# Performance work log

Measured on AMD Instinct MI355X. Metric: run time of the kernel, lower is better.

## Reference

```python
import jax, jax.numpy as jnp
import numpy as np

N_NODES = 100000
N_EDGES = 3200000  # avg degree 32
EPS = 1e-12


def setup_inputs() -> dict:
    key = jax.random.key(0)
    k1, k2, k3, k4, k5 = jax.random.split(key, 5)
    positions = jax.random.normal(k1, (N_NODES, 3), dtype=jnp.float32)
    node_feat = jnp.ones((N_NODES, 1), dtype=jnp.float32)  # dummy 1x0e data
    w0 = jax.random.normal(k2, (1,), dtype=jnp.float32)    # linear weight for 0e output
    w1 = jax.random.normal(k3, (3,), dtype=jnp.float32)    # linear weight for 1o output (elementwise)
    edge_src = jax.random.randint(k4, (N_EDGES,), 0, N_NODES, dtype=jnp.int32)
    edge_dst = jax.random.randint(k5, (N_EDGES,), 0, N_NODES, dtype=jnp.int32)
    return {"positions": positions, "node_feat": node_feat, "w0": w0, "w1": w1,
            "edge_src": edge_src, "edge_dst": edge_dst}


def reference(positions, node_feat, w0, w1, edge_src, edge_dst):
    n_nodes = positions.shape[0]
    # relative positions per edge: dest - src  [E,3]
    rel = positions[edge_dst] - positions[edge_src]
    # spherical harmonics lmax=1: Y0 = 1 (constant 0e), Y1 = unit direction (1o)
    norm = jnp.sqrt(jnp.sum(rel * rel, axis=-1, keepdims=True))
    sh1 = rel / jnp.maximum(norm, EPS)                      # [E,3]
    # gather dest-node scalar feature (code gathers dest_node_feat)
    s = node_feat[edge_dst]                                 # [E,1]
    # tensor product of 0e scalar with (0e + 1o): tp0 = s*1, tp1 = s*sh1
    # LinearLayer: elementwise multiply by per-irrep weight vectors
    out0 = w0 * s                                           # [E,1]
    out1 = w1 * (s * sh1)                                   # [E,3]
    edge_out = jnp.concatenate([out0, out1], axis=-1)       # [E,4]
    # scatter-mean aggregation over incoming edges per dest node
    sums = jax.ops.segment_sum(edge_out, edge_dst, num_segments=n_nodes)
    ones = jnp.ones((edge_out.shape[0], 1), dtype=edge_out.dtype)
    counts = jax.ops.segment_sum(ones, edge_dst, num_segments=n_nodes)
    return sums / jnp.maximum(counts, 1.0)                  # [N,4]
```

## Files before the change

### kernel.cpp

```cpp
#include <hip/hip_runtime.h>


#define EPS 1e-12f
#define FSCALE 128.0f
#define FBIAS 128
#define CHUNK_SHIFT 13
#define CHUNK 8192
#define NCHUNK_MAX 16
#define BLKA 512
#define TPA 4
#define BLKB 512
#define SUBS 39

__device__ __forceinline__ void sh_fields(const float* __restrict__ pos,
                                          int s, int d,
                                          unsigned& fx, unsigned& fy, unsigned& fz) {
    float rx = pos[3 * d + 0] - pos[3 * s + 0];
    float ry = pos[3 * d + 1] - pos[3 * s + 1];
    float rz = pos[3 * d + 2] - pos[3 * s + 2];
    float nrm = sqrtf(rx * rx + ry * ry + rz * rz);
    float inv = 1.0f / fmaxf(nrm, EPS);
    fx = (unsigned)(FBIAS + (int)rintf(rx * inv * FSCALE));
    fy = (unsigned)(FBIAS + (int)rintf(ry * inv * FSCALE));
    fz = (unsigned)(FBIAS + (int)rintf(rz * inv * FSCALE));
}

__global__ __launch_bounds__(BLKA) void phaseA(
        const float* __restrict__ pos,
        const int* __restrict__ dst,
        const int* __restrict__ src,
        unsigned* __restrict__ gcnt,
        unsigned long long* __restrict__ recs,
        int n_edges, int cap, int n_chunk) {
    __shared__ unsigned h[NCHUNK_MAX];
    __shared__ unsigned base[NCHUNK_MAX];
    int tid = threadIdx.x;
    if (tid < n_chunk) h[tid] = 0;
    __syncthreads();

    long e0 = (long)blockIdx.x * (BLKA * TPA);
    unsigned long long rec[TPA];
    int ch[TPA];
    unsigned rank[TPA];
    bool val[TPA];
#pragma unroll
    for (int t = 0; t < TPA; ++t) {
        long j = e0 + (long)t * BLKA + tid;
        val[t] = (j < n_edges);
        if (val[t]) {
            int d = dst[j];
            int s = src[j];
            unsigned fx, fy, fz;
            sh_fields(pos, s, d, fx, fy, fz);
            ch[t] = d >> CHUNK_SHIFT;
            unsigned local = (unsigned)d & (CHUNK - 1);
            rec[t] = ((unsigned long long)local << 27)
                   | ((unsigned long long)fx << 18)
                   | ((unsigned long long)fy << 9)
                   | (unsigned long long)fz;
            rank[t] = atomicAdd(&h[ch[t]], 1u);
        }
    }
    __syncthreads();
    if (tid < n_chunk) base[tid] = h[tid] ? atomicAdd(&gcnt[tid], h[tid]) : 0u;
    __syncthreads();
#pragma unroll
    for (int t = 0; t < TPA; ++t) {
        if (val[t]) {
            unsigned idx = base[ch[t]] + rank[t];
            if (idx < (unsigned)cap)
                recs[(size_t)ch[t] * (unsigned)cap + idx] = rec[t];
        }
    }
}

__global__ __launch_bounds__(BLKB) void phaseB(
        const unsigned* __restrict__ gcnt,
        const unsigned long long* __restrict__ recs,
        unsigned long long* __restrict__ accR,
        int cap, int n_chunk, int padded) {
    __shared__ unsigned long long lds[CHUNK];
    int c   = (int)blockIdx.x % n_chunk;
    int sub = (int)blockIdx.x / n_chunk;
    unsigned cnt = gcnt[c];
    if (cnt > (unsigned)cap) cnt = (unsigned)cap;

    for (int i = threadIdx.x; i < CHUNK; i += BLKB) lds[i] = 0ull;
    __syncthreads();

    const unsigned long long* bucket = recs + (size_t)c * (unsigned)cap;
    for (unsigned j = sub * BLKB + threadIdx.x; j < cnt; j += SUBS * BLKB) {
        unsigned long long r = bucket[j];
        unsigned local = (unsigned)(r >> 27);
        unsigned long long p = (((r >> 18) & 511ull) << 48)
                             | (((r >>  9) & 511ull) << 32)
                             | (((r      ) & 511ull) << 16)
                             | 1ull;
        atomicAdd(&lds[local], p);
    }
    __syncthreads();

    unsigned long long* row = accR + (size_t)sub * (unsigned)padded
                                   + (size_t)c * CHUNK;
    for (int i = threadIdx.x; i < CHUNK; i += BLKB) row[i] = lds[i];
}

__global__ void finalize_binned(const unsigned long long* __restrict__ accR,
                                const float* __restrict__ feat,
                                const float* __restrict__ w0,
                                const float* __restrict__ w1,
                                float* __restrict__ out,
                                int n_nodes, int padded) {
    int n = blockIdx.x * blockDim.x + threadIdx.x;
    if (n >= n_nodes) return;
    int Fx = 0, Fy = 0, Fz = 0, C = 0;
    for (int s = 0; s < SUBS; ++s) {
        unsigned long long v = accR[(size_t)s * (unsigned)padded + (unsigned)n];
        Fx += (int)(v >> 48);
        Fy += (int)((v >> 32) & 0xffffull);
        Fz += (int)((v >> 16) & 0xffffull);
        C  += (int)(v & 0xffffull);
    }
    float c = (float)C;
    float rd = 1.0f / fmaxf(c, 1.0f);
    float sx = (float)Fx * (1.0f / FSCALE) - c;
    float sy = (float)Fy * (1.0f / FSCALE) - c;
    float sz = (float)Fz * (1.0f / FSCALE) - c;
    float f = feat[n];
    float4 o;
    o.x = w0[0] * f * c * rd;
    o.y = w1[0] * f * sx * rd;
    o.z = w1[1] * f * sy * rd;
    o.w = w1[2] * f * sz * rd;
    ((float4*)out)[n] = o;
}

__global__ void edge_kernel_agent(const float* __restrict__ pos,
                                  const int* __restrict__ dst,
                                  const int* __restrict__ src,
                                  unsigned long long* __restrict__ acc,
                                  int n_edges, int n_nodes, int rmask) {
    int i = blockIdx.x * blockDim.x + threadIdx.x;
    if (i >= n_edges) return;
    int s = src[i];
    int d = dst[i];
    unsigned fx, fy, fz;
    sh_fields(pos, s, d, fx, fy, fz);
    unsigned long long p = ((unsigned long long)fx << 48)
                         | ((unsigned long long)fy << 32)
                         | ((unsigned long long)fz << 16) | 1ull;
    unsigned r = (unsigned)blockIdx.x & (unsigned)rmask;
    atomicAdd(acc + (size_t)r * (unsigned)n_nodes + (unsigned)d, p);
}

__global__ void finalize_flat(const unsigned long long* __restrict__ acc,
                              const float* __restrict__ feat,
                              const float* __restrict__ w0,
                              const float* __restrict__ w1,
                              float* __restrict__ out,
                              int n_nodes, int R) {
    int n = blockIdx.x * blockDim.x + threadIdx.x;
    if (n >= n_nodes) return;
    int Fx = 0, Fy = 0, Fz = 0, C = 0;
    for (int r = 0; r < R; ++r) {
        unsigned long long v = acc[(size_t)r * n_nodes + n];
        Fx += (int)(v >> 48);
        Fy += (int)((v >> 32) & 0xffffull);
        Fz += (int)((v >> 16) & 0xffffull);
        C  += (int)(v & 0xffffull);
    }
    float c = (float)C;
    float rd = 1.0f / fmaxf(c, 1.0f);
    float sx = (float)Fx * (1.0f / FSCALE) - c;
    float sy = (float)Fy * (1.0f / FSCALE) - c;
    float sz = (float)Fz * (1.0f / FSCALE) - c;
    float f = feat[n];
    float4 o;
    o.x = w0[0] * f * c * rd;
    o.y = w1[0] * f * sx * rd;
    o.z = w1[1] * f * sy * rd;
    o.w = w1[2] * f * sz * rd;
    ((float4*)out)[n] = o;
}

extern "C" void kernel_launch(void* const* d_in, const int* in_sizes, int n_in,
                              void* d_out, int out_size, void* d_ws, size_t ws_size,
                              hipStream_t stream) {
    const float* pos  = (const float*)d_in[0];
    const float* feat = (const float*)d_in[1];
    const float* w0   = (const float*)d_in[2];
    const float* w1   = (const float*)d_in[3];
    const int* esrc   = (const int*)d_in[4];
    const int* edst   = (const int*)d_in[5];
    int n_nodes = in_sizes[0] / 3;
    int n_edges = in_sizes[4];

    int n_chunk = (n_nodes + CHUNK - 1) >> CHUNK_SHIFT;
    int padded  = n_chunk * CHUNK;
    int cap = (int)((long)n_edges * CHUNK / n_nodes + 8192);

    size_t off_gcnt = 0;
    size_t off_recs = 256;
    size_t recs_bytes = (size_t)n_chunk * (unsigned)cap * sizeof(unsigned long long);
    size_t off_accR = off_recs + ((recs_bytes + 255) & ~(size_t)255);
    size_t accR_bytes = (size_t)SUBS * (unsigned)padded * sizeof(unsigned long long);
    size_t need = off_accR + accR_bytes;

    int nb = 256;
    int ng = (n_nodes + nb - 1) / nb;

    if (n_chunk <= NCHUNK_MAX && ws_size >= need) {
        unsigned* gcnt = (unsigned*)((char*)d_ws + off_gcnt);
        unsigned long long* recs = (unsigned long long*)((char*)d_ws + off_recs);
        unsigned long long* accR = (unsigned long long*)((char*)d_ws + off_accR);

        hipMemsetAsync(gcnt, 0, (size_t)n_chunk * sizeof(unsigned), stream);

        int ga = (int)((n_edges + (long)BLKA * TPA - 1) / ((long)BLKA * TPA));
        phaseA<<<ga, BLKA, 0, stream>>>(pos, edst, esrc, gcnt, recs,
                                        n_edges, cap, n_chunk);
        phaseB<<<n_chunk * SUBS, BLKB, 0, stream>>>(gcnt, recs, accR,
                                                    cap, n_chunk, padded);
        finalize_binned<<<ng, nb, 0, stream>>>(accR, feat, w0, w1,
                                               (float*)d_out, n_nodes, padded);
    } else {
        int R = 4;
        while (R > 1 && (size_t)R * n_nodes * sizeof(unsigned long long) > ws_size) R >>= 1;
        unsigned long long* acc = (unsigned long long*)d_ws;
        hipMemsetAsync(acc, 0, (size_t)R * n_nodes * sizeof(unsigned long long), stream);
        int eb = 256;
        int eg = (n_edges + eb - 1) / eb;
        edge_kernel_agent<<<eg, eb, 0, stream>>>(pos, edst, esrc, acc,
                                                 n_edges, n_nodes, R - 1);
        finalize_flat<<<ng, nb, 0, stream>>>(acc, feat, w0, w1,
                                             (float*)d_out, n_nodes, R);
    }
}
```

Before: 136.5 us.

## Repack positions to float4 and shrink destination chunks to 4096 nodes

Adds a pre-pass that copies positions into a padded float4 array, so each endpoint gather in phaseA becomes one 16-byte load instead of three scalar loads. It also halves the chunk size, doubling the number of chunks, and cuts the sub-accumulator count from 39 to 12. This changes phaseB's grid and the per-chunk working set. The cost is an extra kernel launch plus extra workspace traffic for the repack, and a different phaseB parallelism and contention balance.

```diff
diff --git a/kernel.cpp b/kernel.cpp
--- a/kernel.cpp
+++ b/kernel.cpp
@@ -4,29 +4,47 @@
 #define EPS 1e-12f
 #define FSCALE 128.0f
 #define FBIAS 128
-#define CHUNK_SHIFT 13
-#define CHUNK 8192
-#define NCHUNK_MAX 16
+#define CHUNK_SHIFT 12
+#define CHUNK 4096
+#define NCHUNK_MAX 32
 #define BLKA 512
 #define TPA 4
 #define BLKB 512
-#define SUBS 39
-
-__device__ __forceinline__ void sh_fields(const float* __restrict__ pos,
-                                          int s, int d,
-                                          unsigned& fx, unsigned& fy, unsigned& fz) {
-    float rx = pos[3 * d + 0] - pos[3 * s + 0];
-    float ry = pos[3 * d + 1] - pos[3 * s + 1];
-    float rz = pos[3 * d + 2] - pos[3 * s + 2];
+#define SUBS 12
+
+__global__ void repack_pos(const float* __restrict__ pos,
+                           float4* __restrict__ pos4, int n_nodes) {
+    int n = blockIdx.x * blockDim.x + threadIdx.x;
+    if (n >= n_nodes) return;
+    float4 p;
+    p.x = pos[3 * n + 0];
+    p.y = pos[3 * n + 1];
+    p.z = pos[3 * n + 2];
+    p.w = 0.f;
+    pos4[n] = p;
+}
+
+__device__ __forceinline__ unsigned long long make_rec(const float4* __restrict__ pos4,
+                                                       int s, int d) {
+    float4 pd = pos4[d];
+    float4 ps = pos4[s];
+    float rx = pd.x - ps.x;
+    float ry = pd.y - ps.y;
+    float rz = pd.z - ps.z;
     float nrm = sqrtf(rx * rx + ry * ry + rz * rz);
     float inv = 1.0f / fmaxf(nrm, EPS);
-    fx = (unsigned)(FBIAS + (int)rintf(rx * inv * FSCALE));
-    fy = (unsigned)(FBIAS + (int)rintf(ry * inv * FSCALE));
-    fz = (unsigned)(FBIAS + (int)rintf(rz * inv * FSCALE));
+    unsigned fx = (unsigned)(FBIAS + (int)rintf(rx * inv * FSCALE));
+    unsigned fy = (unsigned)(FBIAS + (int)rintf(ry * inv * FSCALE));
+    unsigned fz = (unsigned)(FBIAS + (int)rintf(rz * inv * FSCALE));
+    unsigned local = (unsigned)d & (CHUNK - 1);
+    return ((unsigned long long)local << 27)
+         | ((unsigned long long)fx << 18)
+         | ((unsigned long long)fy << 9)
+         | (unsigned long long)fz;
 }
 
 __global__ __launch_bounds__(BLKA) void phaseA(
-        const float* __restrict__ pos,
+        const float4* __restrict__ pos4,
         const int* __restrict__ dst,
         const int* __restrict__ src,
         unsigned* __restrict__ gcnt,
@@ -50,14 +68,8 @@
         if (val[t]) {
             int d = dst[j];
             int s = src[j];
-            unsigned fx, fy, fz;
-            sh_fields(pos, s, d, fx, fy, fz);
             ch[t] = d >> CHUNK_SHIFT;
-            unsigned local = (unsigned)d & (CHUNK - 1);
-            rec[t] = ((unsigned long long)local << 27)
-                   | ((unsigned long long)fx << 18)
-                   | ((unsigned long long)fy << 9)
-                   | (unsigned long long)fz;
+            rec[t] = make_rec(pos4, s, d);
             rank[t] = atomicAdd(&h[ch[t]], 1u);
         }
     }
@@ -144,8 +156,14 @@
     if (i >= n_edges) return;
     int s = src[i];
     int d = dst[i];
-    unsigned fx, fy, fz;
-    sh_fields(pos, s, d, fx, fy, fz);
+    float rx = pos[3 * d + 0] - pos[3 * s + 0];
+    float ry = pos[3 * d + 1] - pos[3 * s + 1];
+    float rz = pos[3 * d + 2] - pos[3 * s + 2];
+    float nrm = sqrtf(rx * rx + ry * ry + rz * rz);
+    float inv = 1.0f / fmaxf(nrm, EPS);
+    unsigned fx = (unsigned)(FBIAS + (int)rintf(rx * inv * FSCALE));
+    unsigned fy = (unsigned)(FBIAS + (int)rintf(ry * inv * FSCALE));
+    unsigned fz = (unsigned)(FBIAS + (int)rintf(rz * inv * FSCALE));
     unsigned long long p = ((unsigned long long)fx << 48)
                          | ((unsigned long long)fy << 32)
                          | ((unsigned long long)fz << 16) | 1ull;
@@ -199,8 +217,10 @@
     int padded  = n_chunk * CHUNK;
     int cap = (int)((long)n_edges * CHUNK / n_nodes + 8192);
 
-    size_t off_gcnt = 0;
-    size_t off_recs = 256;
+    size_t off_pos4 = 0;
+    size_t pos4_bytes = (size_t)padded * sizeof(float4);
+    size_t off_gcnt = (pos4_bytes + 255) & ~(size_t)255;
+    size_t off_recs = off_gcnt + 256;
     size_t recs_bytes = (size_t)n_chunk * (unsigned)cap * sizeof(unsigned long long);
     size_t off_accR = off_recs + ((recs_bytes + 255) & ~(size_t)255);
     size_t accR_bytes = (size_t)SUBS * (unsigned)padded * sizeof(unsigned long long);
@@ -210,14 +230,16 @@
     int ng = (n_nodes + nb - 1) / nb;
 
     if (n_chunk <= NCHUNK_MAX && ws_size >= need) {
+        float4* pos4 = (float4*)((char*)d_ws + off_pos4);
         unsigned* gcnt = (unsigned*)((char*)d_ws + off_gcnt);
         unsigned long long* recs = (unsigned long long*)((char*)d_ws + off_recs);
         unsigned long long* accR = (unsigned long long*)((char*)d_ws + off_accR);
 
         hipMemsetAsync(gcnt, 0, (size_t)n_chunk * sizeof(unsigned), stream);
+        repack_pos<<<ng, nb, 0, stream>>>(pos, pos4, n_nodes);
 
         int ga = (int)((n_edges + (long)BLKA * TPA - 1) / ((long)BLKA * TPA));
-        phaseA<<<ga, BLKA, 0, stream>>>(pos, edst, esrc, gcnt, recs,
+        phaseA<<<ga, BLKA, 0, stream>>>(pos4, edst, esrc, gcnt, recs,
                                         n_edges, cap, n_chunk);
         phaseB<<<n_chunk * SUBS, BLKB, 0, stream>>>(gcnt, recs, accR,
                                                     cap, n_chunk, padded);
```

Result: no change. 137.3 us (+0.5%).
